# Optimization experiments

Measured on AMD Instinct MI355X. Metric: run time of the kernel, lower is better.

Reference implementation:

```python
import jax, jax.numpy as jnp
import numpy as np

DIM = 2048
N_HEADS = 16
N_KV = 4
HEAD_DIM = DIM // N_HEADS  # 128
B, S = 2, 2048
EPS = float(np.finfo(np.float32).eps)  # torch RMSNorm eps=None -> finfo eps


def _rotate_half(x):
    # interleaved-pair rotation: out[..., ::2] = -x[..., 1::2]; out[..., 1::2] = x[..., ::2]
    x2 = x.reshape(x.shape[:-1] + (HEAD_DIM // 2, 2))
    rot = jnp.stack([-x2[..., 1], x2[..., 0]], axis=-1)
    return rot.reshape(x.shape)


def _rmsnorm(x, w):
    var = jnp.mean(x * x, axis=-1, keepdims=True)
    return x * jax.lax.rsqrt(var + EPS) * w


def setup_inputs() -> dict:
    key = jax.random.key(0)
    ks = jax.random.split(key, 5)
    out_f = (N_HEADS + 2 * N_KV) * HEAD_DIM  # 3072
    return {
        "x": jax.random.normal(ks[0], (B, S, DIM), jnp.float32),
        "wqkv": jax.random.normal(ks[1], (out_f, DIM), jnp.float32) * (2.0 / (DIM + out_f)) ** 0.5,
        "wo": jax.random.normal(ks[2], (DIM, DIM), jnp.float32) * (1.0 / DIM) ** 0.5,
        "q_norm_w": jnp.ones((HEAD_DIM,), jnp.float32),
        "k_norm_w": jnp.ones((HEAD_DIM,), jnp.float32),
        "freqs_cos": jnp.cos(jax.random.normal(ks[3], (S, 1, HEAD_DIM), jnp.float32)),
        "freqs_sin": jnp.sin(jax.random.normal(ks[4], (S, 1, HEAD_DIM), jnp.float32)),
    }


def reference(x, wqkv, wo, q_norm_w, k_norm_w, freqs_cos, freqs_sin):
    b, s, _ = x.shape
    qkv = jnp.einsum("bsd,od->bso", x, wqkv)
    q_size = N_HEADS * HEAD_DIM
    kv_size = N_KV * HEAD_DIM
    xq = qkv[..., :q_size].reshape(b, s, N_HEADS, HEAD_DIM)
    xk = qkv[..., q_size:q_size + kv_size].reshape(b, s, N_KV, HEAD_DIM)
    xv = qkv[..., q_size + kv_size:].reshape(b, s, N_KV, HEAD_DIM)
    xq = _rmsnorm(xq, q_norm_w)
    xk = _rmsnorm(xk, k_norm_w)
    # RoPE (freqs broadcast over batch and heads)
    xq = xq * freqs_cos + _rotate_half(xq) * freqs_sin
    xk = xk * freqs_cos + _rotate_half(xk) * freqs_sin
    # GQA: group query heads per kv head instead of materializing repeats
    rep = N_HEADS // N_KV
    q = xq.transpose(0, 2, 1, 3).reshape(b, N_KV, rep, s, HEAD_DIM)
    k = xk.transpose(0, 2, 1, 3)  # [b, kv, s, d]
    v = xv.transpose(0, 2, 1, 3)
    scale = 1.0 / jnp.sqrt(jnp.asarray(HEAD_DIM, x.dtype))
    scores = jnp.einsum("bhgqd,bhkd->bhgqk", q, k) * scale
    probs = jax.nn.softmax(scores, axis=-1)
    attn = jnp.einsum("bhgqk,bhkd->bhgqd", probs, v)
    attn = attn.reshape(b, N_HEADS, s, HEAD_DIM).transpose(0, 2, 1, 3).reshape(b, s, DIM)
    return jnp.einsum("bsd,od->bso", attn, wo)
```

## Files before the change

### kernel.cpp

```cpp
#include <hip/hip_runtime.h>
#include <hip/hip_bf16.h>

typedef unsigned short u16;
typedef __bf16 bf16x8 __attribute__((ext_vector_type(8)));
typedef __bf16 bf16x4 __attribute__((ext_vector_type(4)));
typedef u16 u16x8 __attribute__((ext_vector_type(8)));
typedef float f32x4 __attribute__((ext_vector_type(4)));
typedef float f32x16 __attribute__((ext_vector_type(16)));

__device__ __forceinline__ u16 f2bf(float f) {
    unsigned u = __float_as_uint(f);
    return (u16)((u + 0x7fffu + ((u >> 16) & 1u)) >> 16);
}
__device__ __forceinline__ unsigned pkbf2(float a, float b) {
    __hip_bfloat162 h = __float22bfloat162_rn(make_float2(a, b));
    return *(unsigned*)&h;
}

__device__ __forceinline__ void gload16(const u16* g, u16* l) {
    __builtin_amdgcn_global_load_lds(
        (const __attribute__((address_space(1))) void*)g,
        (__attribute__((address_space(3))) void*)l, 16, 0, 0);
}

__device__ __forceinline__ void block_sync() {
    __builtin_amdgcn_sched_barrier(0);
    __builtin_amdgcn_s_barrier();
    __builtin_amdgcn_sched_barrier(0);
}
template<int N> __device__ __forceinline__ void waitvm() {
    if constexpr (N == 0)      asm volatile("s_waitcnt vmcnt(0)" ::: "memory");
    else if constexpr (N == 4) asm volatile("s_waitcnt vmcnt(4)" ::: "memory");
    else if constexpr (N == 6) asm volatile("s_waitcnt vmcnt(6)" ::: "memory");
    else                       asm volatile("s_waitcnt vmcnt(8)" ::: "memory");
}

#define CVT_N1 2097152
#define CVT_N2 3670016
#define CVT_TOT 4718592
__global__ void cvt_all(const float* __restrict__ x, const float* __restrict__ wqkv,
                        const float* __restrict__ wo, u16* __restrict__ xb,
                        u16* __restrict__ wqkvb, u16* __restrict__ wob) {
    for (int i = blockIdx.x * 256 + threadIdx.x; i < CVT_TOT; i += 4608 * 256) {
        const float* s; u16* d; int j;
        if (i < CVT_N1)      { s = x;    d = xb;    j = i; }
        else if (i < CVT_N2) { s = wqkv; d = wqkvb; j = i - CVT_N1; }
        else                 { s = wo;   d = wob;   j = i - CVT_N2; }
        float4 v = *(const float4*)(s + (size_t)j * 4);
        uint2 o; o.x = pkbf2(v.x, v.y); o.y = pkbf2(v.z, v.w);
        *(uint2*)(d + (size_t)j * 4) = o;
    }
}

template<int ROWS>
__device__ __forceinline__ void stage_tile(const u16* __restrict__ g, int K,
                                           int k0, u16* l, int tid) {
#pragma unroll
    for (int s = 0; s < ROWS / 64; ++s) {
        int row = s * 64 + (tid >> 3);
        int sc = (tid & 7) ^ ((tid >> 3) & 7);
        gload16(g + (size_t)row * K + k0 + sc * 8, l + s * 4096 + tid * 8);
    }
}

template<int BM, int BN>
__device__ __forceinline__ void gemm_pipeline(const u16* __restrict__ Ab,
                                              const u16* __restrict__ Bb, int K,
                                              u16* sAll,
                                              f32x4 (&acc)[BM / 32][BN / 64],
                                              int tid) {
    constexpr int MR = BM / 32, NR = BN / 64;
    constexpr int TILE = (BM + BN) * 64;
    const int lane = tid & 63, wave = tid >> 6;
    const int quad = lane >> 4, l16 = lane & 15;
    const int wm = wave >> 2, wn = wave & 3;
    const int ar0 = wm * (BM / 2) + l16;
    const int br0 = wn * (BN / 4) + l16;

    u16* sA0 = sAll;        u16* sB0 = sAll + BM * 64;
    u16* sA1 = sAll + TILE; u16* sB1 = sAll + TILE + BM * 64;

    stage_tile<BM>(Ab, K, 0, sA0, tid);
    stage_tile<BN>(Bb, K, 0, sB0, tid);

    const int nt = K >> 6;
    for (int t = 0; t < nt; ++t) {
        const u16* cA = (t & 1) ? sA1 : sA0;
        const u16* cB = (t & 1) ? sB1 : sB0;
        if (t + 1 < nt) {
            u16* nA = (t & 1) ? sA0 : sA1;
            u16* nB = (t & 1) ? sB0 : sB1;
            stage_tile<BM>(Ab, K, (t + 1) * 64, nA, tid);
            stage_tile<BN>(Bb, K, (t + 1) * 64, nB, tid);
            waitvm<(BM + BN) / 64>();
        } else {
            waitvm<0>();
        }
        block_sync();
#pragma unroll
        for (int kk = 0; kk < 2; ++kk) {
            const int c = kk * 4 + quad;
            bf16x8 af[MR], bf[NR];
#pragma unroll
            for (int m = 0; m < MR; ++m) {
                int r = ar0 + m * 16;
                af[m] = *(const bf16x8*)&cA[r * 64 + ((c ^ (r & 7)) * 8)];
            }
#pragma unroll
            for (int n = 0; n < NR; ++n) {
                int r = br0 + n * 16;
                bf[n] = *(const bf16x8*)&cB[r * 64 + ((c ^ (r & 7)) * 8)];
            }
            __builtin_amdgcn_s_setprio(1);
#pragma unroll
            for (int m = 0; m < MR; ++m)
#pragma unroll
                for (int n = 0; n < NR; ++n)
                    acc[m][n] = __builtin_amdgcn_mfma_f32_16x16x32_bf16(
                        af[m], bf[n], acc[m][n], 0, 0, 0);
            __builtin_amdgcn_s_setprio(0);
        }
        block_sync();
    }
}

__global__ __launch_bounds__(512, 2)
void gemm_bt(const u16* __restrict__ A, const u16* __restrict__ B,
             float* __restrict__ C, int M, int N, int K) {
    __shared__ u16 sAll[2 * (128 + 256) * 64];
    const int tid = threadIdx.x;
    const int wave = tid >> 6, lane = tid & 63;
    const int quad = lane >> 4, l16 = lane & 15;
    const int wm = wave >> 2, wn = wave & 3;
    const int bid = blockIdx.x;
    const int xcd = bid & 7, r2 = bid >> 3;
    const int bni = (xcd & 1) * 4 + (r2 & 3);
    const int bmi = (xcd >> 1) * 8 + (r2 >> 2);
    const size_t bm = (size_t)bmi * 128, bn = (size_t)bni * 256;
    f32x4 acc[4][4] = {};
    gemm_pipeline<128, 256>(A + bm * K, B + bn * K, K, sAll, acc, tid);
#pragma unroll
    for (int m = 0; m < 4; ++m)
#pragma unroll
        for (int n = 0; n < 4; ++n)
#pragma unroll
            for (int r = 0; r < 4; ++r)
                C[(bm + wm * 64 + m * 16 + quad * 4 + r) * (size_t)N +
                  bn + wn * 64 + n * 16 + l16] = acc[m][n][r];
}

__global__ __launch_bounds__(512, 2)
void gemm_qkv(const u16* __restrict__ xb, const u16* __restrict__ wq,
              const float* __restrict__ qw, const float* __restrict__ kw,
              const float* __restrict__ fcos, const float* __restrict__ fsin,
              u16* __restrict__ qb, u16* __restrict__ kb, u16* __restrict__ vt) {
    __shared__ u16 sAll[2 * (256 + 256) * 64];
    const int tid = threadIdx.x;
    const int wave = tid >> 6, lane = tid & 63;
    const int quad = lane >> 4, l16 = lane & 15;
    const int wm = wave >> 2, wn = wave & 3;
    const int bid = blockIdx.x;
    const int xcd = bid & 7, r2 = bid >> 3;
    const int bx = (xcd & 1) * 6 + r2 % 6;
    const int by = (xcd >> 1) * 4 + r2 / 6;
    f32x4 acc[8][4] = {};
    gemm_pipeline<256, 256>(xb + (size_t)by * 256 * 2048,
                            wq + (size_t)bx * 256 * 2048, 2048, sAll, acc, tid);

    const int b = by >> 3;
    const int sb = (by & 7) * 256 + wm * 128;
    const int headh = wn >> 1;
    const int dcol0 = (wn & 1) * 64;

    if (bx >= 10) {
        const int qp = ((quad & 1) << 1) | (quad >> 1);
        const int kvh = (bx - 10) * 2 + headh;
        u16* base = vt + (size_t)(b * 4 + kvh) * 128 * 2048;
#pragma unroll
        for (int m = 0; m < 8; ++m) {
            int s0 = sb + m * 16 + qp * 4;
#pragma unroll
            for (int n = 0; n < 4; ++n) {
                int d = dcol0 + n * 16 + l16;
                bf16x4 pv;
#pragma unroll
                for (int r = 0; r < 4; ++r) pv[r] = (__bf16)acc[m][n][r];
                *(bf16x4*)(base + (size_t)d * 2048 + s0) = pv;
            }
        }
        return;
    }

    float* red = (float*)sAll;
    float ssq[8][4];
#pragma unroll
    for (int m = 0; m < 8; ++m)
#pragma unroll
        for (int r = 0; r < 4; ++r) {
            float t = 0.f;
#pragma unroll
            for (int n = 0; n < 4; ++n) t += acc[m][n][r] * acc[m][n][r];
#pragma unroll
            for (int off = 1; off <= 8; off <<= 1) t += __shfl_xor(t, off);
            ssq[m][r] = t;
        }
    if (l16 == 0)
#pragma unroll
        for (int m = 0; m < 8; ++m)
#pragma unroll
            for (int r = 0; r < 4; ++r)
                red[((wn & 1) * 2 + headh) * 256 + wm * 128 + m * 16 + quad * 4 + r] =
                    ssq[m][r];
    __syncthreads();

    const bool isQ = bx < 8;
    const float qscl = isQ ? 0.08838834764831845f * 1.4426950408889634f : 1.0f;
    const float* wp = isQ ? qw : kw;
    float wcol[4];
#pragma unroll
    for (int n = 0; n < 4; ++n) wcol[n] = wp[dcol0 + n * 16 + l16];
    u16* dstbase = isQ ? qb + (size_t)(b * 16 + bx * 2 + headh) * 2048 * 128
                       : kb + (size_t)(b * 4 + (bx - 8) * 2 + headh) * 2048 * 128;
    const float sgn = (l16 & 1) ? 1.f : -1.f;

#pragma unroll
    for (int m = 0; m < 8; ++m) {
#pragma unroll
        for (int r = 0; r < 4; ++r) {
            int rowl = wm * 128 + m * 16 + quad * 4 + r;
            float var = (red[(0 + headh) * 256 + rowl] +
                         red[(2 + headh) * 256 + rowl]) * (1.0f / 128.0f);
            float rms = rsqrtf(var + 1.1920928955078125e-07f) * qscl;
            int s = sb + m * 16 + quad * 4 + r;
            const float* fc = fcos + (size_t)s * 128 + dcol0;
            const float* fn = fsin + (size_t)s * 128 + dcol0;
            u16* drow = dstbase + (size_t)s * 128 + dcol0;
#pragma unroll
            for (int n = 0; n < 4; ++n) {
                float y = acc[m][n][r] * rms * wcol[n];
                float yp = __shfl_xor(y, 1);
                float o = y * fc[n * 16 + l16] + sgn * yp * fn[n * 16 + l16];
                drow[n * 16 + l16] = f2bf(o);
            }
        }
    }
}

#define KBUF(c) ((c) * 8192)
#define VBUF 16384
__global__ __launch_bounds__(256, 3)
void flash_attn(const u16* __restrict__ qb, const u16* __restrict__ kb,
                const u16* __restrict__ vt, u16* __restrict__ ab) {
    __shared__ u16 smem[24576];
    __shared__ float Llds[128];

    const int tid = threadIdx.x;
    const int wave = tid >> 6, lane = tid & 63;
    const int hf = lane >> 5, c32 = lane & 31;
    const int bid = blockIdx.x;
    const int swz = (bid & 7) * 64 + (bid >> 3);
    const int qt = swz & 15, bh = swz >> 4;
    const int hh = bh & 15, bb = bh >> 4;
    const int kh = hh >> 2;

    const u16* Qbase = qb + (size_t)(bb * 16 + hh) * 2048 * 128;
    const u16* Kbase = kb + (size_t)(bb * 4 + kh) * 2048 * 128;
    const u16* Vbase = vt + (size_t)(bb * 4 + kh) * 128 * 2048;

    bf16x8 aq[8];
#pragma unroll
    for (int kq = 0; kq < 8; ++kq)
        aq[kq] = *(const bf16x8*)(Qbase +
            (size_t)(qt * 128 + wave * 32 + c32) * 128 + kq * 16 + hf * 8);

    f32x16 O[4] = {};
    float lacc = 0.f;

    const int krow = tid >> 4;
    const u16* kg = Kbase + (size_t)krow * 128 + (((tid & 15) ^ (krow & 7)) * 8);
    const int vrow = tid >> 3;
    const u16* vg = Vbase + (size_t)vrow * 2048 + (((tid & 7) ^ (vrow & 7)) * 8);

    auto stageK = [&](int buf, int key0) {
#pragma unroll
        for (int s = 0; s < 4; ++s)
            gload16(kg + key0 * 128 + s * 2048, &smem[KBUF(buf) + s * 2048 + tid * 8]);
    };
    auto stageV = [&](int key0) {
#pragma unroll
        for (int s = 0; s < 4; ++s)
            gload16(vg + (size_t)s * 65536 + key0, &smem[VBUF + s * 2048 + tid * 8]);
    };

    stageK(0, 0);
    stageV(0);

    for (int kt = 0; kt < 32; ++kt) {
        const int cur = kt & 1;
        if (kt < 31) {
            stageK(cur ^ 1, (kt + 1) * 64);
            waitvm<8>();
        } else {
            waitvm<0>();
        }
        block_sync();

        f32x16 sc[2] = {};
        __builtin_amdgcn_s_setprio(1);
#pragma unroll
        for (int kq = 0; kq < 8; ++kq) {
#pragma unroll
            for (int mt = 0; mt < 2; ++mt) {
                bf16x8 kf = *(const bf16x8*)&smem[KBUF(cur) + (mt * 32 + c32) * 128 +
                                                 (((kq * 2 + hf) ^ (c32 & 7)) * 8)];
                sc[mt] = __builtin_amdgcn_mfma_f32_32x32x16_bf16(kf, aq[kq], sc[mt], 0, 0, 0);
            }
        }
        __builtin_amdgcn_s_setprio(0);

        int pdw[2][8];
#pragma unroll
        for (int mt = 0; mt < 2; ++mt) {
            float p[16];
#pragma unroll
            for (int r = 0; r < 16; ++r) p[r] = __builtin_amdgcn_exp2f(sc[mt][r]);
            float a0 = (p[0] + p[1]) + (p[2] + p[3]);
            float a1 = (p[4] + p[5]) + (p[6] + p[7]);
            float a2 = (p[8] + p[9]) + (p[10] + p[11]);
            float a3 = (p[12] + p[13]) + (p[14] + p[15]);
            lacc += (a0 + a1) + (a2 + a3);
#pragma unroll
            for (int i = 0; i < 8; ++i) pdw[mt][i] = (int)pkbf2(p[2 * i], p[2 * i + 1]);
        }

        if (kt < 31) waitvm<4>();
        else         waitvm<0>();
        block_sync();

        __builtin_amdgcn_s_setprio(1);
#pragma unroll
        for (int kc = 0; kc < 4; ++kc) {
            const int mt = kc >> 1, L = kc & 1;
            union { int i[4]; bf16x8 v; } u;
            u.i[0] = pdw[mt][4 * L + 0];
            u.i[1] = pdw[mt][4 * L + 1];
            u.i[2] = pdw[mt][4 * L + 2];
            u.i[3] = pdw[mt][4 * L + 3];
#pragma unroll
            for (int dt = 0; dt < 4; ++dt) {
                bf16x8 vf = *(const bf16x8*)&smem[VBUF + (dt * 32 + c32) * 64 +
                                                 (((kc * 2 + hf) ^ (c32 & 7)) * 8)];
                O[dt] = __builtin_amdgcn_mfma_f32_32x32x16_bf16(u.v, vf, O[dt], 0, 0, 0);
            }
        }
        __builtin_amdgcn_s_setprio(0);
        block_sync();
        if (kt < 31) stageV((kt + 1) * 64);
    }

    float l = lacc + __shfl_xor(lacc, 32);
    if (hf == 0) Llds[wave * 32 + c32] = l;

    float inv[16];
#pragma unroll
    for (int r = 0; r < 16; ++r)
        inv[r] = __builtin_amdgcn_rcpf(Llds[wave * 32 + (r & 3) + 8 * (r >> 2) + 4 * hf]);

    u16* scr = &smem[wave * 32 * 136];
#pragma unroll
    for (int dt = 0; dt < 4; ++dt)
#pragma unroll
        for (int r = 0; r < 16; ++r) {
            int q_r = (r & 3) + 8 * (r >> 2) + 4 * hf;
            scr[q_r * 136 + dt * 32 + c32] = f2bf(O[dt][r] * inv[r]);
        }
#pragma unroll
    for (int it = 0; it < 8; ++it) {
        int f = it * 64 + lane;
        int row = f >> 4, c = f & 15;
        u16x8 v = *(const u16x8*)&scr[row * 136 + c * 8];
        int qg = qt * 128 + wave * 32 + row;
        *(u16x8*)(ab + ((size_t)(bb * 2048 + qg)) * 2048 + hh * 128 + c * 8) = v;
    }
}

extern "C" void kernel_launch(void* const* d_in, const int* in_sizes, int n_in,
                              void* d_out, int out_size, void* d_ws, size_t ws_size,
                              hipStream_t stream) {
    const float* x    = (const float*)d_in[0];
    const float* wqkv = (const float*)d_in[1];
    const float* wo   = (const float*)d_in[2];
    const float* qw   = (const float*)d_in[3];
    const float* kw   = (const float*)d_in[4];
    const float* fc   = (const float*)d_in[5];
    const float* fs   = (const float*)d_in[6];
    float* out = (float*)d_out;
    char* ws = (char*)d_ws;

    u16* xb    = (u16*)(ws + 0);
    u16* wqkvb = (u16*)(ws + 16777216);
    u16* wob   = (u16*)(ws + 29360128);
    u16* qb    = (u16*)(ws + 37748736);
    u16* kb    = (u16*)(ws + 54525952);
    u16* vt    = (u16*)(ws + 58720256);
    u16* ab    = (u16*)(ws + 62914560);

    cvt_all<<<4608, 256, 0, stream>>>(x, wqkv, wo, xb, wqkvb, wob);
    gemm_qkv<<<192, 512, 0, stream>>>(xb, wqkvb, qw, kw, fc, fs, qb, kb, vt);
    flash_attn<<<512, 256, 0, stream>>>(qb, kb, vt, ab);
    gemm_bt<<<256, 512, 0, stream>>>(ab, wob, out, 4096, 2048, 2048);
}
```

Before: 300.1 us.

## Switch GEMM mainloop to triple-buffered K=32 tiles with one barrier per step

The shared GEMM pipeline moves from double-buffered 64-wide K tiles with two barriers per iteration to a three-stage ring of 32-wide K tiles. Loads for tile t+2 are issued right after the barrier and waited on with a vmcnt window, leaving one barrier per step. This aims to hide global-load latency better and cut barrier stalls, at the cost of twice as many loop iterations and fewer MFMAs per barrier. A __syncthreads was added before the reduction reuses shared memory, because with a single barrier per step, waves could still be reading the last tile when the scratch area is overwritten.

New measurement: 297.7 us. About the same (-0.8%).

```diff
diff --git a/kernel.cpp b/kernel.cpp
--- a/kernel.cpp
+++ b/kernel.cpp
@@ -30,6 +30,7 @@
 }
 template<int N> __device__ __forceinline__ void waitvm() {
     if constexpr (N == 0)      asm volatile("s_waitcnt vmcnt(0)" ::: "memory");
+    else if constexpr (N == 3) asm volatile("s_waitcnt vmcnt(3)" ::: "memory");
     else if constexpr (N == 4) asm volatile("s_waitcnt vmcnt(4)" ::: "memory");
     else if constexpr (N == 6) asm volatile("s_waitcnt vmcnt(6)" ::: "memory");
     else                       asm volatile("s_waitcnt vmcnt(8)" ::: "memory");
@@ -53,12 +54,12 @@
 }
 
 template<int ROWS>
-__device__ __forceinline__ void stage_tile(const u16* __restrict__ g, int K,
-                                           int k0, u16* l, int tid) {
-#pragma unroll
-    for (int s = 0; s < ROWS / 64; ++s) {
-        int row = s * 64 + (tid >> 3);
-        int sc = (tid & 7) ^ ((tid >> 3) & 7);
+__device__ __forceinline__ void stage32(const u16* __restrict__ g, int K,
+                                        int k0, u16* l, int tid) {
+#pragma unroll
+    for (int s = 0; s < ROWS / 128; ++s) {
+        int row = s * 128 + (tid >> 2);
+        int sc = (tid & 3) ^ ((tid >> 2) & 3);
         gload16(g + (size_t)row * K + k0 + sc * 8, l + s * 4096 + tid * 8);
     }
 }
@@ -70,64 +71,60 @@
                                               f32x4 (&acc)[BM / 32][BN / 64],
                                               int tid) {
     constexpr int MR = BM / 32, NR = BN / 64;
-    constexpr int TILE = (BM + BN) * 64;
+    constexpr int TILE = (BM + BN) * 32;
+    constexpr int NLD = (BM + BN) / 128;
     const int lane = tid & 63, wave = tid >> 6;
     const int quad = lane >> 4, l16 = lane & 15;
     const int wm = wave >> 2, wn = wave & 3;
     const int ar0 = wm * (BM / 2) + l16;
     const int br0 = wn * (BN / 4) + l16;
 
-    u16* sA0 = sAll;        u16* sB0 = sAll + BM * 64;
-    u16* sA1 = sAll + TILE; u16* sB1 = sAll + TILE + BM * 64;
-
-    stage_tile<BM>(Ab, K, 0, sA0, tid);
-    stage_tile<BN>(Bb, K, 0, sB0, tid);
-
-    const int nt = K >> 6;
+    stage32<BM>(Ab, K, 0, sAll, tid);
+    stage32<BN>(Bb, K, 0, sAll + BM * 32, tid);
+    stage32<BM>(Ab, K, 32, sAll + TILE, tid);
+    stage32<BN>(Bb, K, 32, sAll + TILE + BM * 32, tid);
+
+    const int nt = K >> 5;
+    int bufc = 0, bufn = 2;
     for (int t = 0; t < nt; ++t) {
-        const u16* cA = (t & 1) ? sA1 : sA0;
-        const u16* cB = (t & 1) ? sB1 : sB0;
-        if (t + 1 < nt) {
-            u16* nA = (t & 1) ? sA0 : sA1;
-            u16* nB = (t & 1) ? sB0 : sB1;
-            stage_tile<BM>(Ab, K, (t + 1) * 64, nA, tid);
-            stage_tile<BN>(Bb, K, (t + 1) * 64, nB, tid);
-            waitvm<(BM + BN) / 64>();
-        } else {
-            waitvm<0>();
-        }
+        if (t < nt - 1) waitvm<NLD>();
+        else            waitvm<0>();
         block_sync();
-#pragma unroll
-        for (int kk = 0; kk < 2; ++kk) {
-            const int c = kk * 4 + quad;
-            bf16x8 af[MR], bf[NR];
-#pragma unroll
-            for (int m = 0; m < MR; ++m) {
-                int r = ar0 + m * 16;
-                af[m] = *(const bf16x8*)&cA[r * 64 + ((c ^ (r & 7)) * 8)];
-            }
-#pragma unroll
-            for (int n = 0; n < NR; ++n) {
-                int r = br0 + n * 16;
-                bf[n] = *(const bf16x8*)&cB[r * 64 + ((c ^ (r & 7)) * 8)];
-            }
-            __builtin_amdgcn_s_setprio(1);
-#pragma unroll
-            for (int m = 0; m < MR; ++m)
-#pragma unroll
-                for (int n = 0; n < NR; ++n)
-                    acc[m][n] = __builtin_amdgcn_mfma_f32_16x16x32_bf16(
-                        af[m], bf[n], acc[m][n], 0, 0, 0);
-            __builtin_amdgcn_s_setprio(0);
-        }
-        block_sync();
+        if (t + 2 < nt) {
+            u16* nb = sAll + bufn * TILE;
+            stage32<BM>(Ab, K, (t + 2) * 32, nb, tid);
+            stage32<BN>(Bb, K, (t + 2) * 32, nb + BM * 32, tid);
+        }
+        const u16* cA = sAll + bufc * TILE;
+        const u16* cB = cA + BM * 32;
+        bf16x8 af[MR], bf[NR];
+#pragma unroll
+        for (int m = 0; m < MR; ++m) {
+            int r = ar0 + m * 16;
+            af[m] = *(const bf16x8*)&cA[r * 32 + ((quad ^ (r & 3)) * 8)];
+        }
+#pragma unroll
+        for (int n = 0; n < NR; ++n) {
+            int r = br0 + n * 16;
+            bf[n] = *(const bf16x8*)&cB[r * 32 + ((quad ^ (r & 3)) * 8)];
+        }
+        __builtin_amdgcn_s_setprio(1);
+#pragma unroll
+        for (int m = 0; m < MR; ++m)
+#pragma unroll
+            for (int n = 0; n < NR; ++n)
+                acc[m][n] = __builtin_amdgcn_mfma_f32_16x16x32_bf16(
+                    af[m], bf[n], acc[m][n], 0, 0, 0);
+        __builtin_amdgcn_s_setprio(0);
+        bufc = (bufc == 2) ? 0 : bufc + 1;
+        bufn = (bufn == 2) ? 0 : bufn + 1;
     }
 }
 
 __global__ __launch_bounds__(512, 2)
 void gemm_bt(const u16* __restrict__ A, const u16* __restrict__ B,
              float* __restrict__ C, int M, int N, int K) {
-    __shared__ u16 sAll[2 * (128 + 256) * 64];
+    __shared__ u16 sAll[3 * (128 + 256) * 32];
     const int tid = threadIdx.x;
     const int wave = tid >> 6, lane = tid & 63;
     const int quad = lane >> 4, l16 = lane & 15;
@@ -154,7 +151,7 @@
               const float* __restrict__ qw, const float* __restrict__ kw,
               const float* __restrict__ fcos, const float* __restrict__ fsin,
               u16* __restrict__ qb, u16* __restrict__ kb, u16* __restrict__ vt) {
-    __shared__ u16 sAll[2 * (256 + 256) * 64];
+    __shared__ u16 sAll[3 * (256 + 256) * 32];
     const int tid = threadIdx.x;
     const int wave = tid >> 6, lane = tid & 63;
     const int quad = lane >> 4, l16 = lane & 15;
@@ -204,6 +201,7 @@
             for (int off = 1; off <= 8; off <<= 1) t += __shfl_xor(t, off);
             ssq[m][r] = t;
         }
+    __syncthreads();
     if (l16 == 0)
 #pragma unroll
         for (int m = 0; m < 8; ++m)
```
